# Optimization experiments

Hardware: AMD Instinct MI355X
Metric: run time of the kernel (lower is better)

The kernel has to match this reference:

```python
import jax, jax.numpy as jnp
import numpy as np

N_NODES = 75000
N_EDGES = 1200000
IN_FEATS = 64
OUT_FEATS = 64


def setup_inputs() -> dict:
    key = jax.random.key(0)
    k1, k2, k3, k4, k5 = jax.random.split(key, 5)
    feature = jax.random.normal(k1, (N_NODES, IN_FEATS), dtype=jnp.float32)
    src = jax.random.randint(k2, (N_EDGES,), 0, N_NODES, dtype=jnp.int32)
    dst = jax.random.randint(k3, (N_EDGES,), 0, N_NODES, dtype=jnp.int32)
    # degree: in-degree + 1 (clamped >= 1 so sqrt/div are well-defined), float32 node data
    deg = np.bincount(np.asarray(dst), minlength=N_NODES).astype(np.float32) + 1.0
    degree = jnp.asarray(deg)
    W = jax.random.normal(k4, (IN_FEATS, OUT_FEATS), dtype=jnp.float32) * (1.0 / np.sqrt(IN_FEATS))
    b = jax.random.normal(k5, (OUT_FEATS,), dtype=jnp.float32) * 0.01
    return {"feature": feature, "degree": degree, "src": src, "dst": dst, "W": W, "b": b}


def reference(feature, degree, src, dst, W, b):
    # message: m_e = h[src_e] / sqrt(degree[src_e])   -> [E, F]
    inv_sqrt_deg = 1.0 / jnp.sqrt(degree)
    m = feature[src] * inv_sqrt_deg[src][:, None]
    # reduce: sum messages into destination nodes      -> [N, F]
    agg = jax.ops.segment_sum(m, dst, num_segments=feature.shape[0])
    # node apply: h = (agg / sqrt(degree)) @ W + b     -> [N, O]
    h = agg * inv_sqrt_deg[:, None]
    return h @ W + b
```

## Files before the change

kernel.cpp:

```cpp
#include <hip/hip_runtime.h>

#define FEATS 64
#define PSZ   64
#define MAXP  1280
#define PSCH  2344
#define SPT   512
#define PEPT  5
#define NBMAX 512
#define CAPP  2560

typedef __attribute__((ext_vector_type(8))) short short8;
typedef __attribute__((ext_vector_type(4))) float floatx4;

static __device__ __forceinline__ unsigned short f2bf(float f) {
    const unsigned int u = __float_as_uint(f);
    return (unsigned short)((u + 0x7FFFu + ((u >> 16) & 1u)) >> 16);
}
static __device__ __forceinline__ float bflo(unsigned int u) {
    return __uint_as_float(u << 16);
}
static __device__ __forceinline__ float bfhi(unsigned int u) {
    return __uint_as_float(u & 0xFFFF0000u);
}

__global__ __launch_bounds__(SPT) void prep_scatter(
        const float* __restrict__ degree,
        const float* __restrict__ feature,
        const float* __restrict__ Wm,
        const int* __restrict__ src,
        const int* __restrict__ dst,
        unsigned short* __restrict__ Fs16,
        unsigned short* __restrict__ WtB,
        int* __restrict__ slab,
        unsigned short* __restrict__ runoff,
        int n_nodes, int n_edges, int np, int rows_per) {
    __shared__ int cnt[MAXP];
    __shared__ int swt[8];
    __shared__ __align__(16) int sval[PSCH];
    const int tid = threadIdx.x;
    const int lane = tid & 63;
    const int wv = tid >> 6;
    const int b = blockIdx.x;

    for (int i = tid; i < np; i += SPT) cnt[i] = 0;

    {
        const int r0 = b * rows_per;
        const int r1 = min(r0 + rows_per, n_nodes);
        const float4* f4 = (const float4*)feature;
        uint4* o4 = (uint4*)Fs16;
        for (int ch = r0 * 8 + tid; ch < r1 * 8; ch += SPT) {
            const float w = rsqrtf(degree[ch >> 3]);
            const float4 fa = f4[ch * 2];
            const float4 fb = f4[ch * 2 + 1];
            uint4 o;
            o.x = (unsigned int)f2bf(fa.x * w) | ((unsigned int)f2bf(fa.y * w) << 16);
            o.y = (unsigned int)f2bf(fa.z * w) | ((unsigned int)f2bf(fa.w * w) << 16);
            o.z = (unsigned int)f2bf(fb.x * w) | ((unsigned int)f2bf(fb.y * w) << 16);
            o.w = (unsigned int)f2bf(fb.z * w) | ((unsigned int)f2bf(fb.w * w) << 16);
            o4[ch] = o;
        }
        if (b == 0) {
            if (tid < FEATS) Fs16[(size_t)n_nodes * FEATS + tid] = 0;
            for (int idx = tid; idx < FEATS * FEATS; idx += SPT) {
                const int k = idx >> 6, n = idx & 63;
                WtB[n * FEATS + k] = f2bf(Wm[idx]);
            }
        }
    }
    __syncthreads();

    const int estart = b * PSCH;
    const int eend = min(estart + PSCH, n_edges);
    const int mb = eend - estart;

    int prk[PEPT];
#pragma unroll
    for (int k = 0; k < PEPT; ++k) {
        const int e = estart + tid + k * SPT;
        prk[k] = 0;
        if (e < eend) {
            const int d = dst[e];
            const int p = d >> 6;
            const int r = atomicAdd(&cnt[p], 1);
            prk[k] = p | (r << 11) | ((d & 63) << 23);
        }
    }
    __syncthreads();

    int my[3];
    int psum = 0;
    const int p0 = tid * 3;
#pragma unroll
    for (int j = 0; j < 3; ++j) {
        const int p = p0 + j;
        my[j] = psum;
        if (p < np) psum += cnt[p];
    }
    int x = psum;
#pragma unroll
    for (int off = 1; off < 64; off <<= 1) {
        const int v = __shfl_up(x, off);
        if (lane >= off) x += v;
    }
    if (lane == 63) swt[wv] = x;
    __syncthreads();
    int wbase = 0;
#pragma unroll
    for (int w = 0; w < 8; ++w) if (w < wv) wbase += swt[w];
    const int tbase = wbase + (x - psum);
#pragma unroll
    for (int j = 0; j < 3; ++j) {
        const int p = p0 + j;
        if (p < np) cnt[p] = tbase + my[j];
    }
    __syncthreads();

#pragma unroll
    for (int k = 0; k < PEPT; ++k) {
        const int e = estart + tid + k * SPT;
        if (e < eend) {
            const int pr = prk[k];
            const int p = pr & 2047;
            const int r = (pr >> 11) & 4095;
            const int dl = (pr >> 23) & 63;
            sval[cnt[p] + r] = (src[e] & 0x1FFFF) | (dl << 17);
        }
    }
    __syncthreads();

    int* so = slab + estart;
    const int m4 = mb >> 2;
    int4* so4 = (int4*)so;
    const int4* sv4 = (const int4*)sval;
    for (int i = tid; i < m4; i += SPT) so4[i] = sv4[i];
    for (int i = (m4 << 2) + tid; i < mb; i += SPT) so[i] = sval[i];
    unsigned short* ro = runoff + (size_t)b * (np + 1);
    for (int i = tid; i <= np; i += SPT)
        ro[i] = (unsigned short)((i < np) ? cnt[i] : mb);
}

__global__ __launch_bounds__(256) void gather_apply5(
        const int* __restrict__ slab,
        const unsigned short* __restrict__ runoff,
        const float* __restrict__ degree,
        const unsigned short* __restrict__ Fs16,
        const unsigned short* __restrict__ WtB,
        const float* __restrict__ bias,
        float* __restrict__ out,
        int n_nodes, int np, int nbs) {
    __shared__ __align__(16) int ledges[CAPP];
    __shared__ __align__(16) unsigned short saggb[PSZ * 72];
    __shared__ int boffA[PSZ + 1];
    __shared__ int bcnt[PSZ];
    __shared__ int bcur[PSZ];
    __shared__ float swinv[PSZ];

    const int tid = threadIdx.x;
    const int lane = tid & 63;
    const int wv = tid >> 6;
    const int p = blockIdx.x;
    const int n0 = p * PSZ;
    const int nn = min(PSZ, n_nodes - n0);

    if (tid < PSZ) bcur[tid] = 0;
    if (wv == 0) {
        const float dg = (lane < nn) ? degree[n0 + lane] : 1.0f;
        swinv[lane] = rsqrtf(dg);
        const int c = (lane < nn) ? ((int)(dg + 0.5f) - 1) : 0;
        const int cp = (c + 7) & ~7;
        int x = cp;
#pragma unroll
        for (int off = 1; off < 64; off <<= 1) {
            const int v = __shfl_up(x, off);
            if (lane >= off) x += v;
        }
        if (lane == 0) boffA[0] = 0;
        boffA[lane + 1] = x;
        bcnt[lane] = c;
    }
    __syncthreads();
    const int mpad = boffA[PSZ];

    if (mpad <= CAPP) {
        for (int i = tid; i < mpad; i += 256) ledges[i] = n_nodes;
        __syncthreads();
        for (int rr = tid; rr < nbs; rr += 256) {
            const unsigned short* ro = runoff + (size_t)rr * (np + 1);
            const int st = ro[p];
            const int en = ro[p + 1];
            const int* g = slab + (size_t)rr * PSCH;
            for (int q = st; q < en; ++q) {
                const int rec = g[q];
                const int dl = (rec >> 17) & 63;
                const int pos = boffA[dl] + atomicAdd(&bcur[dl], 1);
                ledges[pos] = rec & 0x1FFFF;
            }
        }
        __syncthreads();

        const int q8 = lane >> 3;
        const int c8 = lane & 7;
        const uint4* FsU4 = (const uint4*)Fs16;
        for (int n = wv; n < PSZ; n += 4) {
            const int st = boffA[n];
            const int en8 = boffA[n + 1];
            float a0 = 0.f, a1 = 0.f, a2 = 0.f, a3 = 0.f;
            float a4 = 0.f, a5 = 0.f, a6 = 0.f, a7 = 0.f;
#pragma unroll 2
            for (int j = st; j < en8; j += 8) {
                const int r = ledges[j + q8];
                const uint4 u = FsU4[((size_t)r << 3) + c8];
                a0 += bflo(u.x); a1 += bfhi(u.x);
                a2 += bflo(u.y); a3 += bfhi(u.y);
                a4 += bflo(u.z); a5 += bfhi(u.z);
                a6 += bflo(u.w); a7 += bfhi(u.w);
            }
#define FOLD(v) v += __shfl_xor(v, 8); v += __shfl_xor(v, 16); v += __shfl_xor(v, 32)
            FOLD(a0); FOLD(a1); FOLD(a2); FOLD(a3);
            FOLD(a4); FOLD(a5); FOLD(a6); FOLD(a7);
#undef FOLD
            if (q8 == 0) {
                uint4 o;
                o.x = (unsigned int)f2bf(a0) | ((unsigned int)f2bf(a1) << 16);
                o.y = (unsigned int)f2bf(a2) | ((unsigned int)f2bf(a3) << 16);
                o.z = (unsigned int)f2bf(a4) | ((unsigned int)f2bf(a5) << 16);
                o.w = (unsigned int)f2bf(a6) | ((unsigned int)f2bf(a7) << 16);
                *(uint4*)(saggb + n * 72 + c8 * 8) = o;
            }
        }
    } else {
        __syncthreads();
        __syncthreads();
        for (int n = wv; n < PSZ; n += 4) {
            float acc = 0.f;
            for (int t = 0; t < nbs; ++t) {
                const unsigned short* ro = runoff + (size_t)t * (np + 1);
                const int gb = t * PSCH;
                const int e0 = ro[p + 1];
                for (int i = ro[p]; i < e0; ++i) {
                    const int rec = slab[gb + i];
                    if (((rec >> 17) & 63) == n) {
                        const unsigned int us =
                            Fs16[((size_t)(rec & 0x1FFFF) << 6) + lane];
                        acc += __uint_as_float(us << 16);
                    }
                }
            }
            saggb[n * 72 + lane] = f2bf(acc);
        }
    }
    __syncthreads();

    const int col = lane & 15;
    const int quad = lane >> 4;
    floatx4 acc[4] = {};
#pragma unroll
    for (int kt = 0; kt < 2; ++kt) {
        const short8 af = *(const short8*)(saggb + (wv * 16 + col) * 72 + kt * 32 + quad * 8);
#pragma unroll
        for (int nt = 0; nt < 4; ++nt) {
            const short8 bf = *(const short8*)((const short*)WtB + (nt * 16 + col) * FEATS + kt * 32 + quad * 8);
            acc[nt] = __builtin_amdgcn_mfma_f32_16x16x32_bf16(af, bf, acc[nt], 0, 0, 0);
        }
    }
#pragma unroll
    for (int nt = 0; nt < 4; ++nt) {
        const float bv = bias[nt * 16 + col];
#pragma unroll
        for (int r = 0; r < 4; ++r) {
            const int row = wv * 16 + quad * 4 + r;
            if (row < nn)
                out[(size_t)(n0 + row) * FEATS + nt * 16 + col] = swinv[row] * acc[nt][r] + bv;
        }
    }
}

static inline size_t align256(size_t x) { return (x + 255) & ~(size_t)255; }

extern "C" void kernel_launch(void* const* d_in, const int* in_sizes, int n_in,
                              void* d_out, int out_size, void* d_ws, size_t ws_size,
                              hipStream_t stream) {
    const float* feature = (const float*)d_in[0];
    const float* degree  = (const float*)d_in[1];
    const int*   src     = (const int*)d_in[2];
    const int*   dst     = (const int*)d_in[3];
    const float* Wm      = (const float*)d_in[4];
    const float* bias    = (const float*)d_in[5];
    float* out = (float*)d_out;

    const int n_nodes = in_sizes[1];
    const int n_edges = in_sizes[2];
    const int np = (n_nodes + PSZ - 1) / PSZ;
    const int nbs = (n_edges + PSCH - 1) / PSCH;
    const int rows_per = (n_nodes + nbs - 1) / nbs;

    char* ws = (char*)d_ws;
    unsigned short* Fs16 = (unsigned short*)ws; ws += align256(((size_t)n_nodes + 1) * FEATS * 2);
    unsigned short* WtB  = (unsigned short*)ws; ws += align256((size_t)FEATS * FEATS * 2);
    int* slab = (int*)ws;                       ws += align256((size_t)nbs * PSCH * 4);
    unsigned short* runoff = (unsigned short*)ws; ws += align256((size_t)nbs * (np + 1) * 2);

    prep_scatter<<<nbs, SPT, 0, stream>>>(degree, feature, Wm, src, dst,
                                          Fs16, WtB, slab, runoff,
                                          n_nodes, n_edges, np, rows_per);
    gather_apply5<<<np, 256, 0, stream>>>(slab, runoff, degree, Fs16, WtB, bias, out,
                                          n_nodes, np, nbs);
}
```

Baseline: 136.4 us.

## Halve scatter chunk size, double gather block to 512 threads with 16-edge unroll

Halves the per-block edge chunk in the scatter stage, which doubles the number of scatter blocks and slab segments. The gather kernel grows to 512 threads with 8 waves per node block. Each wave now loads two feature rows per iteration, so edge lists are padded to multiples of 16, and the MFMA output tile is split so each wave computes half of a 16-row tile. The aim is more memory-level parallelism and occupancy in the gather. The cost is more padding rows (dummy loads) and more runoff entries scanned per gather block, since nbs doubles.

```diff
diff --git a/kernel.cpp b/kernel.cpp
--- a/kernel.cpp
+++ b/kernel.cpp
@@ -3,10 +3,9 @@
 #define FEATS 64
 #define PSZ   64
 #define MAXP  1280
-#define PSCH  2344
+#define PSCH  1172
 #define SPT   512
-#define PEPT  5
-#define NBMAX 512
+#define PEPT  3
 #define CAPP  2560
 
 typedef __attribute__((ext_vector_type(8))) short short8;
@@ -140,7 +139,7 @@
         ro[i] = (unsigned short)((i < np) ? cnt[i] : mb);
 }
 
-__global__ __launch_bounds__(256) void gather_apply5(
+__global__ __launch_bounds__(512, 8) void gather_apply6(
         const int* __restrict__ slab,
         const unsigned short* __restrict__ runoff,
         const float* __restrict__ degree,
@@ -152,7 +151,6 @@
     __shared__ __align__(16) int ledges[CAPP];
     __shared__ __align__(16) unsigned short saggb[PSZ * 72];
     __shared__ int boffA[PSZ + 1];
-    __shared__ int bcnt[PSZ];
     __shared__ int bcur[PSZ];
     __shared__ float swinv[PSZ];
 
@@ -168,7 +166,7 @@
         const float dg = (lane < nn) ? degree[n0 + lane] : 1.0f;
         swinv[lane] = rsqrtf(dg);
         const int c = (lane < nn) ? ((int)(dg + 0.5f) - 1) : 0;
-        const int cp = (c + 7) & ~7;
+        const int cp = (c + 15) & ~15;
         int x = cp;
 #pragma unroll
         for (int off = 1; off < 64; off <<= 1) {
@@ -177,15 +175,14 @@
         }
         if (lane == 0) boffA[0] = 0;
         boffA[lane + 1] = x;
-        bcnt[lane] = c;
     }
     __syncthreads();
     const int mpad = boffA[PSZ];
 
     if (mpad <= CAPP) {
-        for (int i = tid; i < mpad; i += 256) ledges[i] = n_nodes;
+        for (int i = tid; i < mpad; i += SPT) ledges[i] = n_nodes;
         __syncthreads();
-        for (int rr = tid; rr < nbs; rr += 256) {
+        for (int rr = tid; rr < nbs; rr += SPT) {
             const unsigned short* ro = runoff + (size_t)rr * (np + 1);
             const int st = ro[p];
             const int en = ro[p + 1];
@@ -202,19 +199,25 @@
         const int q8 = lane >> 3;
         const int c8 = lane & 7;
         const uint4* FsU4 = (const uint4*)Fs16;
-        for (int n = wv; n < PSZ; n += 4) {
+        for (int n = wv; n < PSZ; n += 8) {
             const int st = boffA[n];
-            const int en8 = boffA[n + 1];
+            const int en16 = boffA[n + 1];
             float a0 = 0.f, a1 = 0.f, a2 = 0.f, a3 = 0.f;
             float a4 = 0.f, a5 = 0.f, a6 = 0.f, a7 = 0.f;
 #pragma unroll 2
-            for (int j = st; j < en8; j += 8) {
-                const int r = ledges[j + q8];
-                const uint4 u = FsU4[((size_t)r << 3) + c8];
-                a0 += bflo(u.x); a1 += bfhi(u.x);
-                a2 += bflo(u.y); a3 += bfhi(u.y);
-                a4 += bflo(u.z); a5 += bfhi(u.z);
-                a6 += bflo(u.w); a7 += bfhi(u.w);
+            for (int j = st; j < en16; j += 16) {
+                const int r0 = ledges[j + q8];
+                const int r1 = ledges[j + 8 + q8];
+                const uint4 u0 = FsU4[((size_t)r0 << 3) + c8];
+                const uint4 u1 = FsU4[((size_t)r1 << 3) + c8];
+                a0 += bflo(u0.x); a1 += bfhi(u0.x);
+                a2 += bflo(u0.y); a3 += bfhi(u0.y);
+                a4 += bflo(u0.z); a5 += bfhi(u0.z);
+                a6 += bflo(u0.w); a7 += bfhi(u0.w);
+                a0 += bflo(u1.x); a1 += bfhi(u1.x);
+                a2 += bflo(u1.y); a3 += bfhi(u1.y);
+                a4 += bflo(u1.z); a5 += bfhi(u1.z);
+                a6 += bflo(u1.w); a7 += bfhi(u1.w);
             }
 #define FOLD(v) v += __shfl_xor(v, 8); v += __shfl_xor(v, 16); v += __shfl_xor(v, 32)
             FOLD(a0); FOLD(a1); FOLD(a2); FOLD(a3);
@@ -232,7 +235,7 @@
     } else {
         __syncthreads();
         __syncthreads();
-        for (int n = wv; n < PSZ; n += 4) {
+        for (int n = wv; n < PSZ; n += 8) {
             float acc = 0.f;
             for (int t = 0; t < nbs; ++t) {
                 const unsigned short* ro = runoff + (size_t)t * (np + 1);
@@ -254,24 +257,28 @@
 
     const int col = lane & 15;
     const int quad = lane >> 4;
-    floatx4 acc[4] = {};
+    const int mt = wv >> 1;
+    const int nh = (wv & 1) << 1;
+    floatx4 acc[2] = {};
 #pragma unroll
     for (int kt = 0; kt < 2; ++kt) {
-        const short8 af = *(const short8*)(saggb + (wv * 16 + col) * 72 + kt * 32 + quad * 8);
-#pragma unroll
-        for (int nt = 0; nt < 4; ++nt) {
+        const short8 af = *(const short8*)(saggb + (mt * 16 + col) * 72 + kt * 32 + quad * 8);
+#pragma unroll
+        for (int t = 0; t < 2; ++t) {
+            const int nt = nh + t;
             const short8 bf = *(const short8*)((const short*)WtB + (nt * 16 + col) * FEATS + kt * 32 + quad * 8);
-            acc[nt] = __builtin_amdgcn_mfma_f32_16x16x32_bf16(af, bf, acc[nt], 0, 0, 0);
-        }
-    }
-#pragma unroll
-    for (int nt = 0; nt < 4; ++nt) {
+            acc[t] = __builtin_amdgcn_mfma_f32_16x16x32_bf16(af, bf, acc[t], 0, 0, 0);
+        }
+    }
+#pragma unroll
+    for (int t = 0; t < 2; ++t) {
+        const int nt = nh + t;
         const float bv = bias[nt * 16 + col];
 #pragma unroll
         for (int r = 0; r < 4; ++r) {
-            const int row = wv * 16 + quad * 4 + r;
+            const int row = mt * 16 + quad * 4 + r;
             if (row < nn)
-                out[(size_t)(n0 + row) * FEATS + nt * 16 + col] = swinv[row] * acc[nt][r] + bv;
+                out[(size_t)(n0 + row) * FEATS + nt * 16 + col] = swinv[row] * acc[t][r] + bv;
         }
     }
 }
@@ -304,6 +311,6 @@
     prep_scatter<<<nbs, SPT, 0, stream>>>(degree, feature, Wm, src, dst,
                                           Fs16, WtB, slab, runoff,
                                           n_nodes, n_edges, np, rows_per);
-    gather_apply5<<<np, 256, 0, stream>>>(slab, runoff, degree, Fs16, WtB, bias, out,
+    gather_apply6<<<np, SPT, 0, stream>>>(slab, runoff, degree, Fs16, WtB, bias, out,
                                           n_nodes, np, nbs);
 }
```

Measured after the change: 134.8 us. About the same (-1.1%).
